# Kernel optimization log

Hardware: AMD Instinct MI355X
Metric: run time of the kernel (lower is better)

## Reference

```python
import jax, jax.numpy as jnp
import numpy as np

D_MODEL = 1024
HEADS = 16
DIM_HEAD = 64
INNER = HEADS * DIM_HEAD


def setup_inputs() -> dict:
    key = jax.random.key(0)
    ks = jax.random.split(key, 5)
    B, N = 4, 2048
    x = jax.random.normal(ks[0], (B, N, D_MODEL), dtype=jnp.float32)
    w_qkv = jax.random.normal(ks[1], (INNER * 3, D_MODEL), dtype=jnp.float32) * (1.0 / np.sqrt(D_MODEL))
    b_qkv = jax.random.normal(ks[2], (INNER * 3,), dtype=jnp.float32) * 0.02
    w_out = jax.random.normal(ks[3], (D_MODEL, INNER), dtype=jnp.float32) * (1.0 / np.sqrt(INNER))
    logit_scale = jnp.log(10.0 * jnp.ones((HEADS, 1, 1), dtype=jnp.float32))
    return {"x": x, "w_qkv": w_qkv, "b_qkv": b_qkv, "w_out": w_out, "logit_scale": logit_scale}


def _l2norm(t, eps=1e-12):
    # matches F.normalize(dim=-1): x / max(||x||, eps)
    n = jnp.sqrt(jnp.sum(t * t, axis=-1, keepdims=True))
    return t / jnp.maximum(n, eps)


def reference(x, w_qkv, b_qkv, w_out, logit_scale):
    B, N, C = x.shape
    qkv = x @ w_qkv.T + b_qkv                      # [B,N,3*INNER]
    qkv = qkv.reshape(B, N, 3, HEADS, DIM_HEAD)
    qkv = jnp.transpose(qkv, (2, 0, 3, 1, 4))       # [3,B,H,N,Dh]
    q, k, v = qkv[0], qkv[1], qkv[2]
    attn = jnp.einsum('bhnd,bhmd->bhnm', _l2norm(q), _l2norm(k))
    scale = jnp.exp(jnp.minimum(logit_scale, jnp.log(1.0 / 0.01)))  # [H,1,1]
    attn = attn * scale[None]                       # broadcast over batch
    attn = jax.nn.softmax(attn, axis=-1)
    out = jnp.einsum('bhnm,bhmd->bhnd', attn, v)    # [B,H,N,Dh]
    out = jnp.transpose(out, (0, 2, 1, 3)).reshape(B, N, C)
    return out @ w_out.T
```

## Files before the change

kernel.cpp:

```cpp
#include <hip/hip_runtime.h>

typedef __attribute__((ext_vector_type(8))) __bf16 bf16x8;
typedef __attribute__((ext_vector_type(4))) float f32x4;
typedef unsigned short u16;

__device__ __forceinline__ u16 f2bf(float f) {
    union { float f; unsigned u; } v; v.f = f;
    unsigned r = v.u + 0x7FFFu + ((v.u >> 16) & 1u);
    return (u16)(r >> 16);
}
__device__ __forceinline__ float bf2f(u16 h) {
    union { unsigned u; float f; } v; v.u = ((unsigned)h) << 16;
    return v.f;
}
__device__ __forceinline__ u16 f2bf_n(float f) {
    union { __bf16 b; u16 u; } t; t.b = (__bf16)f; return t.u;
}
__device__ __forceinline__ bf16x8 ld_bf16x8(const u16* p) {
    union { uint4 u; bf16x8 b; } t;
    t.u = *(const uint4*)p;
    return t.b;
}
__device__ __forceinline__ void async16(const void* g, const void* l) {
    __builtin_amdgcn_global_load_lds((const __attribute__((address_space(1))) void*)g,
                                     (__attribute__((address_space(3))) void*)l, 16, 0, 0);
}

#define BATCH 4
#define NSEQ 2048
#define HEADS 16
#define DH 64
#define DMODEL 1024
#define MROWS 8192
#define NQKV 3072

__global__ void split_bf16(const float* __restrict__ src, u16* __restrict__ hi,
                           u16* __restrict__ lo, int n) {
    int i = blockIdx.x * blockDim.x + threadIdx.x;
    if (i < n) {
        float f = src[i];
        u16 h = f2bf(f);
        hi[i] = h;
        lo[i] = f2bf(f - bf2f(h));
    }
}
__global__ void cvt_bf16(const float* __restrict__ src, u16* __restrict__ dst, int n) {
    int i = blockIdx.x * blockDim.x + threadIdx.x;
    if (i < n) dst[i] = f2bf(src[i]);
}

__global__ __launch_bounds__(256) void qkv_gemm(
    const u16* __restrict__ A,
    const u16* __restrict__ Bh, const u16* __restrict__ Bl,
    const float* __restrict__ bias,
    u16* __restrict__ Qn, u16* __restrict__ Kn, u16* __restrict__ Vt) {
    const int K = DMODEL, TK = 32;
    __shared__ __align__(16) u16 sA[128 * 32];
    __shared__ __align__(16) u16 sBh[128 * 32], sBl[128 * 32];
    const int tid = threadIdx.x, wave = tid >> 6, lane = tid & 63;
    const int quad = lane >> 4, l16 = lane & 15;
    const int m0 = blockIdx.x * 128, n0 = blockIdx.y * 128;
    const int wm = (wave & 1) * 64, wn = (wave >> 1) * 64;
    f32x4 acc[4][4] = {};

    for (int k0 = 0; k0 < K; k0 += TK) {
        __syncthreads();
        #pragma unroll
        for (int pass = 0; pass < 2; ++pass) {
            const int c = pass * 256 + tid;
            const int row = c >> 2, part = c & 3;
            const int ldsOff = (pass * 256 + wave * 64) * 16;
            const size_t ga = (size_t)(m0 + row) * K + k0 + part * 8;
            const size_t gb = (size_t)(n0 + row) * K + k0 + part * 8;
            async16(A + ga, (const char*)sA + ldsOff);
            async16(Bh + gb, (const char*)sBh + ldsOff);
            async16(Bl + gb, (const char*)sBl + ldsOff);
        }
        __syncthreads();
        bf16x8 a[4];
        #pragma unroll
        for (int mt = 0; mt < 4; ++mt)
            a[mt] = ld_bf16x8(&sA[(wm + mt * 16 + l16) * TK + quad * 8]);
        #pragma unroll
        for (int nt = 0; nt < 4; ++nt) {
            const int cix = wn + nt * 16 + l16;
            bf16x8 bh = ld_bf16x8(&sBh[cix * TK + quad * 8]);
            bf16x8 bl = ld_bf16x8(&sBl[cix * TK + quad * 8]);
            #pragma unroll
            for (int mt = 0; mt < 4; ++mt) {
                acc[mt][nt] = __builtin_amdgcn_mfma_f32_16x16x32_bf16(a[mt], bh, acc[mt][nt], 0, 0, 0);
                acc[mt][nt] = __builtin_amdgcn_mfma_f32_16x16x32_bf16(a[mt], bl, acc[mt][nt], 0, 0, 0);
            }
        }
    }

    #pragma unroll
    for (int nt = 0; nt < 4; ++nt) {
        const float bv = bias[n0 + wn + nt * 16 + l16];
        #pragma unroll
        for (int mt = 0; mt < 4; ++mt)
            #pragma unroll
            for (int r = 0; r < 4; ++r)
                acc[mt][nt][r] += bv;
    }

    if (n0 < 2048) {
        u16* dst = (n0 < 1024) ? Qn : Kn;
        const int nq = (n0 & 1023) + wn;
        const int hh = nq >> 6;
        #pragma unroll
        for (int mt = 0; mt < 4; ++mt) {
            float ss[4] = {};
            #pragma unroll
            for (int nt = 0; nt < 4; ++nt)
                #pragma unroll
                for (int r = 0; r < 4; ++r)
                    ss[r] += acc[mt][nt][r] * acc[mt][nt][r];
            #pragma unroll
            for (int r = 0; r < 4; ++r) {
                ss[r] += __shfl_xor(ss[r], 1);
                ss[r] += __shfl_xor(ss[r], 2);
                ss[r] += __shfl_xor(ss[r], 4);
                ss[r] += __shfl_xor(ss[r], 8);
                ss[r] = 1.f / fmaxf(sqrtf(ss[r]), 1e-12f);
            }
            const int mbase = m0 + wm + mt * 16 + quad * 4;
            const int b = mbase >> 11, n = mbase & 2047;
            #pragma unroll
            for (int r = 0; r < 4; ++r) {
                size_t rowoff = (((size_t)(b * HEADS + hh)) * NSEQ + n + r) * DH;
                #pragma unroll
                for (int nt = 0; nt < 4; ++nt)
                    dst[rowoff + nt * 16 + l16] = f2bf_n(acc[mt][nt][r] * ss[r]);
            }
        }
    } else {
        const int nv = (n0 - 2048) + wn;
        const int hh = nv >> 6;
        #pragma unroll
        for (int nt = 0; nt < 4; ++nt) {
            const int d = (nv & 63) + nt * 16 + l16;
            #pragma unroll
            for (int mt = 0; mt < 4; ++mt) {
                const int mbase = m0 + wm + mt * 16 + quad * 4;
                const int b = mbase >> 11, n = mbase & 2047;
                ushort4 t;
                t.x = f2bf_n(acc[mt][nt][0]);
                t.y = f2bf_n(acc[mt][nt][1]);
                t.z = f2bf_n(acc[mt][nt][2]);
                t.w = f2bf_n(acc[mt][nt][3]);
                *(ushort4*)&Vt[(((size_t)(b * HEADS + hh)) * DH + d) * NSEQ + n] = t;
            }
        }
    }
}

__global__ __launch_bounds__(256) void out_gemm(
    const u16* __restrict__ A, const u16* __restrict__ B, float* __restrict__ C) {
    const int K = DMODEL, N = DMODEL, TK = 32;
    __shared__ __align__(16) u16 sA[128 * 32], sB[128 * 32];
    const int tid = threadIdx.x, wave = tid >> 6, lane = tid & 63;
    const int quad = lane >> 4, l16 = lane & 15;
    const int m0 = blockIdx.x * 128, n0 = blockIdx.y * 128;
    const int wm = (wave & 1) * 64, wn = (wave >> 1) * 64;
    f32x4 acc[4][4] = {};

    for (int k0 = 0; k0 < K; k0 += TK) {
        __syncthreads();
        #pragma unroll
        for (int pass = 0; pass < 2; ++pass) {
            const int c = pass * 256 + tid;
            const int row = c >> 2, part = c & 3;
            const int ldsOff = (pass * 256 + wave * 64) * 16;
            const size_t ga = (size_t)(m0 + row) * K + k0 + part * 8;
            const size_t gb = (size_t)(n0 + row) * K + k0 + part * 8;
            async16(A + ga, (const char*)sA + ldsOff);
            async16(B + gb, (const char*)sB + ldsOff);
        }
        __syncthreads();
        bf16x8 a[4];
        #pragma unroll
        for (int mt = 0; mt < 4; ++mt)
            a[mt] = ld_bf16x8(&sA[(wm + mt * 16 + l16) * TK + quad * 8]);
        #pragma unroll
        for (int nt = 0; nt < 4; ++nt) {
            bf16x8 b = ld_bf16x8(&sB[(wn + nt * 16 + l16) * TK + quad * 8]);
            #pragma unroll
            for (int mt = 0; mt < 4; ++mt)
                acc[mt][nt] = __builtin_amdgcn_mfma_f32_16x16x32_bf16(a[mt], b, acc[mt][nt], 0, 0, 0);
        }
    }
    #pragma unroll
    for (int nt = 0; nt < 4; ++nt) {
        const int n = n0 + wn + nt * 16 + l16;
        #pragma unroll
        for (int mt = 0; mt < 4; ++mt) {
            const int mbase = m0 + wm + mt * 16 + quad * 4;
            #pragma unroll
            for (int r = 0; r < 4; ++r)
                C[(size_t)(mbase + r) * N + n] = acc[mt][nt][r];
        }
    }
}

__global__ __launch_bounds__(256) void flash_attn(
    const u16* __restrict__ Q, const u16* __restrict__ Kn, const u16* __restrict__ Vt,
    const float* __restrict__ lsc, u16* __restrict__ AO) {
    const int bh = blockIdx.x;
    const int q0 = blockIdx.y * 64;
    const int h = bh & (HEADS - 1), b = bh >> 4;
    const int tid = threadIdx.x, wave = tid >> 6, lane = tid & 63;
    const int quad = lane >> 4, l16 = lane & 15;
    const float scale = __expf(fminf(lsc[h], 4.6051702f));
    const float c1 = scale * 1.4426950408889634f;

    __shared__ __align__(16) u16 Ks[64][72];
    __shared__ __align__(16) u16 Vs[64][72];
    __shared__ __align__(16) u16 Ps[4][16][68];

    const u16* qbase = Q + ((size_t)bh * NSEQ + q0 + wave * 16) * DH;
    bf16x8 qa[2];
    qa[0] = ld_bf16x8(qbase + l16 * DH + quad * 8);
    qa[1] = ld_bf16x8(qbase + l16 * DH + 32 + quad * 8);

    f32x4 O[4] = {};
    float lr[4] = {0.f, 0.f, 0.f, 0.f};

    const u16* kb = Kn + (size_t)bh * NSEQ * DH;
    const u16* vb = Vt + (size_t)bh * DH * NSEQ;

    for (int kt = 0; kt < NSEQ; kt += 64) {
        __syncthreads();
        #pragma unroll
        for (int c = tid; c < 512; c += 256) {
            int key = c >> 3, part = c & 7;
            *(uint4*)&Ks[key][part * 8] = *(const uint4*)(kb + (size_t)(kt + key) * DH + part * 8);
        }
        #pragma unroll
        for (int c = tid; c < 512; c += 256) {
            int d = c >> 3, part = c & 7;
            *(uint4*)&Vs[d][part * 8] = *(const uint4*)(vb + (size_t)d * NSEQ + kt + part * 8);
        }
        __syncthreads();

        f32x4 S[4] = {};
        #pragma unroll
        for (int nt = 0; nt < 4; ++nt) {
            bf16x8 k0 = ld_bf16x8(&Ks[nt * 16 + l16][quad * 8]);
            bf16x8 k1 = ld_bf16x8(&Ks[nt * 16 + l16][32 + quad * 8]);
            S[nt] = __builtin_amdgcn_mfma_f32_16x16x32_bf16(qa[0], k0, S[nt], 0, 0, 0);
            S[nt] = __builtin_amdgcn_mfma_f32_16x16x32_bf16(qa[1], k1, S[nt], 0, 0, 0);
        }

        #pragma unroll
        for (int nt = 0; nt < 4; ++nt) {
            #pragma unroll
            for (int r = 0; r < 4; ++r) {
                float pv = __builtin_amdgcn_exp2f(__builtin_fmaf(S[nt][r], c1, -c1));
                lr[r] += pv;
                Ps[wave][quad * 4 + r][nt * 16 + l16] = f2bf_n(pv);
            }
        }
        asm volatile("s_waitcnt lgkmcnt(0)" ::: "memory");
        bf16x8 pa0 = ld_bf16x8(&Ps[wave][l16][quad * 8]);
        bf16x8 pa1 = ld_bf16x8(&Ps[wave][l16][32 + quad * 8]);

        #pragma unroll
        for (int dt = 0; dt < 4; ++dt) {
            bf16x8 v0 = ld_bf16x8(&Vs[dt * 16 + l16][quad * 8]);
            bf16x8 v1 = ld_bf16x8(&Vs[dt * 16 + l16][32 + quad * 8]);
            O[dt] = __builtin_amdgcn_mfma_f32_16x16x32_bf16(pa0, v0, O[dt], 0, 0, 0);
            O[dt] = __builtin_amdgcn_mfma_f32_16x16x32_bf16(pa1, v1, O[dt], 0, 0, 0);
        }
    }

    #pragma unroll
    for (int r = 0; r < 4; ++r) {
        float s = lr[r];
        s += __shfl_xor(s, 1);
        s += __shfl_xor(s, 2);
        s += __shfl_xor(s, 4);
        s += __shfl_xor(s, 8);
        lr[r] = fmaxf(s, 1e-30f);
    }

    #pragma unroll
    for (int r = 0; r < 4; ++r) {
        float inv = 1.f / lr[r];
        size_t row = (size_t)b * NSEQ + q0 + wave * 16 + quad * 4 + r;
        #pragma unroll
        for (int dt = 0; dt < 4; ++dt)
            AO[row * DMODEL + h * DH + dt * 16 + l16] = f2bf_n(O[dt][r] * inv);
    }
}

extern "C" void kernel_launch(void* const* d_in, const int* in_sizes, int n_in,
                              void* d_out, int out_size, void* d_ws, size_t ws_size,
                              hipStream_t stream) {
    const float* x    = (const float*)d_in[0];
    const float* wqkv = (const float*)d_in[1];
    const float* bqkv = (const float*)d_in[2];
    const float* wout = (const float*)d_in[3];
    const float* lsc  = (const float*)d_in[4];

    char* ws = (char*)d_ws;
    u16* xb   = (u16*)(ws + 0);
    u16* wqh  = (u16*)(ws + 16777216);
    u16* wql  = (u16*)(ws + 23068672);
    u16* wob  = (u16*)(ws + 29360128);
    u16* qn   = (u16*)(ws + 31457280);
    u16* kn   = (u16*)(ws + 48234496);
    u16* vt   = (u16*)(ws + 65011712);
    u16* ao   = xb;

    cvt_bf16<<<MROWS * DMODEL / 256, 256, 0, stream>>>(x, xb, MROWS * DMODEL);
    split_bf16<<<NQKV * DMODEL / 256, 256, 0, stream>>>(wqkv, wqh, wql, NQKV * DMODEL);
    cvt_bf16<<<DMODEL * DMODEL / 256, 256, 0, stream>>>(wout, wob, DMODEL * DMODEL);

    qkv_gemm<<<dim3(MROWS / 128, NQKV / 128), 256, 0, stream>>>(xb, wqh, wql, bqkv, qn, kn, vt);
    flash_attn<<<dim3(BATCH * HEADS, NSEQ / 64), 256, 0, stream>>>(qn, kn, vt, lsc, ao);
    out_gemm<<<dim3(MROWS / 128, DMODEL / 128), 256, 0, stream>>>(ao, wob, (float*)d_out);
}
```

Before: 427.7 us.

## Load K/V fragments directly from global into registers in flash attention

The flash attention kernel no longer stages K and V tiles through shared memory behind two block barriers per iteration. Each wave now loads its MFMA operand fragments straight from global memory into registers. An occupancy hint of 4 blocks per CU is added to the launch bounds. This removes the LDS round-trip and the barriers, but each of the four waves now reads the same K/V tile, so global and cache traffic is redundant. The loads are also used right away with no prefetch, which may expose their latency. A redundant `nv & 63` term in the V-transpose store index is also dropped.

```diff
diff --git a/kernel.cpp b/kernel.cpp
--- a/kernel.cpp
+++ b/kernel.cpp
@@ -139,7 +139,7 @@
         const int hh = nv >> 6;
         #pragma unroll
         for (int nt = 0; nt < 4; ++nt) {
-            const int d = (nv & 63) + nt * 16 + l16;
+            const int d = nt * 16 + l16;
             #pragma unroll
             for (int mt = 0; mt < 4; ++mt) {
                 const int mbase = m0 + wm + mt * 16 + quad * 4;
@@ -203,7 +203,7 @@
     }
 }
 
-__global__ __launch_bounds__(256) void flash_attn(
+__global__ __launch_bounds__(256, 4) void flash_attn(
     const u16* __restrict__ Q, const u16* __restrict__ Kn, const u16* __restrict__ Vt,
     const float* __restrict__ lsc, u16* __restrict__ AO) {
     const int bh = blockIdx.x;
@@ -214,8 +214,6 @@
     const float scale = __expf(fminf(lsc[h], 4.6051702f));
     const float c1 = scale * 1.4426950408889634f;
 
-    __shared__ __align__(16) u16 Ks[64][72];
-    __shared__ __align__(16) u16 Vs[64][72];
     __shared__ __align__(16) u16 Ps[4][16][68];
 
     const u16* qbase = Q + ((size_t)bh * NSEQ + q0 + wave * 16) * DH;
@@ -226,30 +224,29 @@
     f32x4 O[4] = {};
     float lr[4] = {0.f, 0.f, 0.f, 0.f};
 
-    const u16* kb = Kn + (size_t)bh * NSEQ * DH;
-    const u16* vb = Vt + (size_t)bh * DH * NSEQ;
+    const u16* kfrag = Kn + (size_t)bh * NSEQ * DH + (size_t)l16 * DH + quad * 8;
+    const u16* vfrag = Vt + (size_t)bh * DH * NSEQ + (size_t)l16 * NSEQ + quad * 8;
 
     for (int kt = 0; kt < NSEQ; kt += 64) {
-        __syncthreads();
-        #pragma unroll
-        for (int c = tid; c < 512; c += 256) {
-            int key = c >> 3, part = c & 7;
-            *(uint4*)&Ks[key][part * 8] = *(const uint4*)(kb + (size_t)(kt + key) * DH + part * 8);
-        }
-        #pragma unroll
-        for (int c = tid; c < 512; c += 256) {
-            int d = c >> 3, part = c & 7;
-            *(uint4*)&Vs[d][part * 8] = *(const uint4*)(vb + (size_t)d * NSEQ + kt + part * 8);
-        }
-        __syncthreads();
+        bf16x8 k0[4], k1[4], v0[4], v1[4];
+        #pragma unroll
+        for (int nt = 0; nt < 4; ++nt) {
+            const u16* p = kfrag + (size_t)(kt + nt * 16) * DH;
+            k0[nt] = ld_bf16x8(p);
+            k1[nt] = ld_bf16x8(p + 32);
+        }
+        #pragma unroll
+        for (int dt = 0; dt < 4; ++dt) {
+            const u16* p = vfrag + (size_t)(dt * 16) * NSEQ + kt;
+            v0[dt] = ld_bf16x8(p);
+            v1[dt] = ld_bf16x8(p + 32);
+        }
 
         f32x4 S[4] = {};
         #pragma unroll
         for (int nt = 0; nt < 4; ++nt) {
-            bf16x8 k0 = ld_bf16x8(&Ks[nt * 16 + l16][quad * 8]);
-            bf16x8 k1 = ld_bf16x8(&Ks[nt * 16 + l16][32 + quad * 8]);
-            S[nt] = __builtin_amdgcn_mfma_f32_16x16x32_bf16(qa[0], k0, S[nt], 0, 0, 0);
-            S[nt] = __builtin_amdgcn_mfma_f32_16x16x32_bf16(qa[1], k1, S[nt], 0, 0, 0);
+            S[nt] = __builtin_amdgcn_mfma_f32_16x16x32_bf16(qa[0], k0[nt], S[nt], 0, 0, 0);
+            S[nt] = __builtin_amdgcn_mfma_f32_16x16x32_bf16(qa[1], k1[nt], S[nt], 0, 0, 0);
         }
 
         #pragma unroll
@@ -267,10 +264,8 @@
 
         #pragma unroll
         for (int dt = 0; dt < 4; ++dt) {
-            bf16x8 v0 = ld_bf16x8(&Vs[dt * 16 + l16][quad * 8]);
-            bf16x8 v1 = ld_bf16x8(&Vs[dt * 16 + l16][32 + quad * 8]);
-            O[dt] = __builtin_amdgcn_mfma_f32_16x16x32_bf16(pa0, v0, O[dt], 0, 0, 0);
-            O[dt] = __builtin_amdgcn_mfma_f32_16x16x32_bf16(pa1, v1, O[dt], 0, 0, 0);
+            O[dt] = __builtin_amdgcn_mfma_f32_16x16x32_bf16(pa0, v0[dt], O[dt], 0, 0, 0);
+            O[dt] = __builtin_amdgcn_mfma_f32_16x16x32_bf16(pa1, v1[dt], O[dt], 0, 0, 0);
         }
     }
 
```

New measurement: 698.7 us. 1.63x slower.
